# Kernel tuning notes

Measured on AMD Instinct MI355X. Metric: run time of the kernel, lower is better.

## Reference

```python
import jax, jax.numpy as jnp
import numpy as np

KERNEL = 5
DILATION = 2
PAD = DILATION * (KERNEL - 1) // 2  # symmetric 'same' padding along the conv axis


def _conv(x, w, b, padding, rhs_dilation):
    y = jax.lax.conv_general_dilated(
        x, w, window_strides=(1, 1), padding=padding,
        rhs_dilation=rhs_dilation,
        dimension_numbers=("NCHW", "OIHW", "NCHW"))
    return y + b[None, :, None, None]


def h_transform(x):
    # shear: [B,C,H,W] -> [B,C,H,2W-1], row i shifted right by i
    B, C, H, W = x.shape
    x = jnp.pad(x, ((0, 0), (0, 0), (0, 0), (0, W)))
    x = x.reshape(B, C, -1)[..., :-W]
    return x.reshape(B, C, H, 2 * W - 1)


def inv_h_transform(x):
    # inverse shear, assumes input [B,C,H,2H-1] -> [B,C,H,H]
    B, C, H, _ = x.shape
    x = x.reshape(B, C, -1)
    x = jnp.pad(x, ((0, 0), (0, 0), (0, H)))
    return x.reshape(B, C, H, 2 * H)[..., :H]


def v_transform(x):
    return jnp.transpose(h_transform(jnp.transpose(x, (0, 1, 3, 2))), (0, 1, 3, 2))


def inv_v_transform(x):
    return jnp.transpose(inv_h_transform(jnp.transpose(x, (0, 1, 3, 2))), (0, 1, 3, 2))


def setup_inputs() -> dict:
    key = jax.random.key(0)
    ks = jax.random.split(key, 9)
    B, C, H, W = 8, 256, 128, 128
    outc = C // 4
    x = jax.random.normal(ks[0], (B, C, H, W), dtype=jnp.float32)
    w_h = jax.random.normal(ks[1], (outc, C, 1, KERNEL), dtype=jnp.float32) * 0.02
    b_h = jax.random.normal(ks[2], (outc,), dtype=jnp.float32) * 0.02
    w_v = jax.random.normal(ks[3], (outc, C, KERNEL, 1), dtype=jnp.float32) * 0.02
    b_v = jax.random.normal(ks[4], (outc,), dtype=jnp.float32) * 0.02
    w_d1 = jax.random.normal(ks[5], (outc, C, KERNEL, 1), dtype=jnp.float32) * 0.02
    b_d1 = jax.random.normal(ks[6], (outc,), dtype=jnp.float32) * 0.02
    w_d2 = jax.random.normal(ks[7], (outc, C, 1, KERNEL), dtype=jnp.float32) * 0.02
    b_d2 = jax.random.normal(ks[8], (outc,), dtype=jnp.float32) * 0.02
    return {"x": x, "w_h": w_h, "b_h": b_h, "w_v": w_v, "b_v": b_v,
            "w_d1": w_d1, "b_d1": b_d1, "w_d2": w_d2, "b_d2": b_d2}


def reference(x, w_h, b_h, w_v, b_v, w_d1, b_d1, w_d2, b_d2):
    # branch 1: horizontal dilated conv (1,k)
    x1 = _conv(x, w_h, b_h, padding=((0, 0), (PAD, PAD)), rhs_dilation=(1, DILATION))
    # branch 2: vertical dilated conv (k,1)
    x2 = _conv(x, w_v, b_v, padding=((PAD, PAD), (0, 0)), rhs_dilation=(DILATION, 1))
    # branch 3: diagonal via h-shear + vertical conv + inverse shear
    x3 = inv_h_transform(_conv(h_transform(x), w_d1, b_d1,
                                padding=((PAD, PAD), (0, 0)), rhs_dilation=(DILATION, 1)))
    # branch 4: anti-diagonal via v-shear + horizontal conv + inverse shear
    x4 = inv_v_transform(_conv(v_transform(x), w_d2, b_d2,
                                padding=((0, 0), (PAD, PAD)), rhs_dilation=(1, DILATION)))
    return jnp.concatenate([x1, x2, x3, x4], axis=1)
```

## Files before the change

kernel.cpp:

```cpp
#include <hip/hip_runtime.h>
#include <hip/hip_bf16.h>


typedef __attribute__((ext_vector_type(8))) __bf16 bf16x8;
typedef __attribute__((ext_vector_type(4))) float f32x4;

#define HH 128
#define WW 128
#define CIN 256
#define NCHUNK 8
#define CHUNK 32
#define COLS 136
#define XS_ELEMS (5*COLS*CHUNK)
#define WPG (40*64*32)

__device__ __forceinline__ ushort f2bf(float f) {
    union { float f; unsigned u; } v; v.f = f;
    unsigned r = v.u + 0x7FFF + ((v.u >> 16) & 1);
    return (ushort)(r >> 16);
}

__global__ void repack_w(const float* __restrict__ w0, const float* __restrict__ w1,
                         const float* __restrict__ w2, const float* __restrict__ w3,
                         ushort* __restrict__ wp) {
    int idx = blockIdx.x * 256 + threadIdx.x;
    int g   = idx / WPG;
    int rem = idx - g * WPG;
    int s   = rem >> 11;
    int r2  = rem & 2047;
    int m   = r2 >> 5;
    int kk  = r2 & 31;
    int k   = s % 5;
    int cc  = s / 5;
    const float* w = (g == 0) ? w0 : (g == 1) ? w1 : (g == 2) ? w2 : w3;
    wp[idx] = f2bf(w[(m * CIN + cc * 32 + kk) * 5 + k]);
}

__global__ __launch_bounds__(256, 4)
void asterisk_mfma(const float* __restrict__ x,
                   const ushort* __restrict__ wp,
                   const float* __restrict__ b0, const float* __restrict__ b1,
                   const float* __restrict__ b2, const float* __restrict__ b3,
                   float* __restrict__ out) {
    __shared__ __align__(16) short xs[XS_ELEMS];

    const int t    = threadIdx.x;
    const int lane = t & 63;
    const int wid  = t >> 6;
    const int m16  = lane & 15;
    const int h    = lane >> 4;

    int id = blockIdx.x;
    int sw = (id & 7) * 128 + (id >> 3);
    const int b = sw >> 7;
    const int i = sw & 127;

    for (int e = t; e < 5 * 8 * CHUNK; e += 256) {
        int r  = e >> 8;
        int pc = (e >> 5) & 7;
        int c  = e & 31;
        int col = (pc < 4) ? pc : 128 + pc;
        xs[(r * COLS + col) * CHUNK + c] = 0;
    }
    for (int r = 0; r < 5; ++r) {
        int row = i + 2 * r - 4;
        if ((unsigned)row >= HH) {
            for (int e = t; e < COLS * CHUNK; e += 256)
                xs[r * COLS * CHUNK + e] = 0;
        }
    }

    const float* bias = (wid == 0) ? b0 : (wid == 1) ? b1 : (wid == 2) ? b2 : b3;
    f32x4 acc[4][8];
#pragma unroll
    for (int mb = 0; mb < 4; ++mb) {
        f32x4 bv;
#pragma unroll
        for (int rr = 0; rr < 4; ++rr) bv[rr] = bias[mb * 16 + h * 4 + rr];
#pragma unroll
        for (int nb = 0; nb < 8; ++nb) acc[mb][nb] = bv;
    }

    const int cg = t >> 5;
    const int q  = t & 31;
    const float* xb = x + (size_t)b * CIN * HH * WW;
    const ushort* wg = wp + (size_t)wid * WPG;

    for (int cc = 0; cc < NCHUNK; ++cc) {
        __syncthreads();
        {
            int c0 = cc * CHUNK + cg * 4;
            int slot = cg >> 1;
            int sub  = (cg & 1) * 4;
            const float* srcc = xb + (size_t)c0 * HH * WW + q * 4;
#pragma unroll
            for (int r = 0; r < 5; ++r) {
                int row = i + 2 * r - 4;
                if ((unsigned)row < HH) {
                    const float* src = srcc + (size_t)row * WW;
                    float4 v0 = *(const float4*)(src);
                    float4 v1 = *(const float4*)(src + HH * WW);
                    float4 v2 = *(const float4*)(src + 2 * HH * WW);
                    float4 v3 = *(const float4*)(src + 3 * HH * WW);
#pragma unroll
                    for (int jj = 0; jj < 4; ++jj) {
                        int col = q * 4 + 4 + jj;
                        int sl  = slot ^ ((col >> 2) & 3);
                        float f0 = ((const float*)&v0)[jj];
                        float f1 = ((const float*)&v1)[jj];
                        float f2 = ((const float*)&v2)[jj];
                        float f3 = ((const float*)&v3)[jj];
                        __hip_bfloat162 lo = __float22bfloat162_rn(make_float2(f0, f1));
                        __hip_bfloat162 hi = __float22bfloat162_rn(make_float2(f2, f3));
                        uint2 pk;
                        pk.x = *(unsigned*)&lo;
                        pk.y = *(unsigned*)&hi;
                        int wi = (r * COLS + col) * CHUNK + sl * 8 + sub;
                        wi ^= ((col >> 4) & 1) << 5;
                        *(uint2*)&xs[wi] = pk;
                    }
                }
            }
        }
        __syncthreads();
        const ushort* wc = wg + (size_t)(cc * 5 * 64 * 32) + m16 * 32 + h * 8;
        bf16x8 a_cur[4], a_nxt[4];
#pragma unroll
        for (int mb = 0; mb < 4; ++mb)
            a_cur[mb] = *(const bf16x8*)(wc + mb * 16 * 32);
#pragma unroll
        for (int k = 0; k < 5; ++k) {
            if (k < 4) {
                const ushort* wk1 = wc + (size_t)(k + 1) * 64 * 32;
#pragma unroll
                for (int mb = 0; mb < 4; ++mb)
                    a_nxt[mb] = *(const bf16x8*)(wk1 + mb * 16 * 32);
            }
            int r  = (wid == 0) ? 2 : (wid == 3 ? 4 - k : k);
            int dj = (wid == 1) ? 0 : (wid == 2 ? 4 - 2 * k : 2 * k - 4);
            int col0 = m16 + dj + 4;
            int sl   = h ^ ((col0 >> 2) & 3);
            int base = (r * COLS + col0) * CHUNK + sl * 8;
            base ^= ((col0 >> 4) & 1) << 5;
#pragma unroll
            for (int nb = 0; nb < 8; ++nb) {
                int idx = (base + nb * 16 * CHUNK) ^ ((nb & 1) << 5);
                bf16x8 bf = *(const bf16x8*)(&xs[idx]);
#pragma unroll
                for (int mb = 0; mb < 4; ++mb)
                    acc[mb][nb] = __builtin_amdgcn_mfma_f32_16x16x32_bf16(
                        a_cur[mb], bf, acc[mb][nb], 0, 0, 0);
            }
            if (k < 4) {
#pragma unroll
                for (int mb = 0; mb < 4; ++mb) a_cur[mb] = a_nxt[mb];
            }
        }
    }

    size_t obase = (((size_t)b * 256 + wid * 64) * HH + i) * WW;
#pragma unroll
    for (int mb = 0; mb < 4; ++mb)
#pragma unroll
        for (int rr = 0; rr < 4; ++rr) {
            float* op = out + obase + (size_t)(mb * 16 + h * 4 + rr) * HH * WW + m16;
#pragma unroll
            for (int nb = 0; nb < 8; ++nb)
                op[nb * 16] = acc[mb][nb][rr];
        }
}

extern "C" void kernel_launch(void* const* d_in, const int* in_sizes, int n_in,
                              void* d_out, int out_size, void* d_ws, size_t ws_size,
                              hipStream_t stream) {
    const float* x    = (const float*)d_in[0];
    const float* w_h  = (const float*)d_in[1];
    const float* b_h  = (const float*)d_in[2];
    const float* w_v  = (const float*)d_in[3];
    const float* b_v  = (const float*)d_in[4];
    const float* w_d1 = (const float*)d_in[5];
    const float* b_d1 = (const float*)d_in[6];
    const float* w_d2 = (const float*)d_in[7];
    const float* b_d2 = (const float*)d_in[8];
    float* out = (float*)d_out;
    ushort* wpack = (ushort*)d_ws;

    repack_w<<<1280, 256, 0, stream>>>(w_h, w_v, w_d1, w_d2, wpack);
    asterisk_mfma<<<1024, 256, 0, stream>>>(x, wpack, b_h, b_v, b_d1, b_d2, out);
}
```

Before: 120.4 us.

## Pre-convert input to swizzled bf16 planes and double-buffer LDS via global_load_lds

Adds a prep kernel that converts x once into bf16 tiles already in the swizzled LDS layout. The main kernel then stages each channel chunk with direct global-to-LDS 16-byte loads into a double buffer, so the next chunk's load overlaps the current chunk's MFMAs. Each 512-thread block computes two output rows that share a 6-row halo instead of 5 rows per single row, which cuts redundant input traffic. The cost is an extra kernel launch plus a full bf16 copy of x written to and read back from the workspace, and the larger block roughly halves the number of workgroups.

```diff
diff --git a/kernel.cpp b/kernel.cpp
--- a/kernel.cpp
+++ b/kernel.cpp
@@ -11,13 +11,22 @@
 #define NCHUNK 8
 #define CHUNK 32
 #define COLS 136
-#define XS_ELEMS (5*COLS*CHUNK)
+#define TROWS 6
+#define BUF_SHORTS (TROWS*COLS*CHUNK)
 #define WPG (40*64*32)
+#define XT_OFF (1u<<20)
+#define XT_BYTES (8u*128u*8u*8192u)
 
 __device__ __forceinline__ ushort f2bf(float f) {
     union { float f; unsigned u; } v; v.f = f;
     unsigned r = v.u + 0x7FFF + ((v.u >> 16) & 1);
     return (ushort)(r >> 16);
+}
+
+__device__ __forceinline__ void gll16(const void* g, const void* l) {
+    __builtin_amdgcn_global_load_lds(
+        (const __attribute__((address_space(1))) unsigned*)g,
+        (__attribute__((address_space(3))) unsigned*)l, 16, 0, 0);
 }
 
 __global__ void repack_w(const float* __restrict__ w0, const float* __restrict__ w1,
@@ -36,25 +45,179 @@
     wp[idx] = f2bf(w[(m * CIN + cc * 32 + kk) * 5 + k]);
 }
 
+__global__ void prep_x(const float* __restrict__ x, ushort* __restrict__ xt) {
+    int plane = blockIdx.x;
+    int cc  = plane & 7;
+    int row = (plane >> 3) & 127;
+    int b   = plane >> 10;
+    ushort* P = xt + (size_t)plane * 4096;
+    const float* xb = x + (((size_t)b * CIN + cc * CHUNK) * HH + row) * WW;
+    int t = threadIdx.x;
+#pragma unroll
+    for (int it = 0; it < 4; ++it) {
+        int id  = t + it * 256;
+        int c   = (id >> 7) * 4;
+        int col = id & 127;
+        float f0 = xb[(size_t)(c + 0) * (HH*WW) + col];
+        float f1 = xb[(size_t)(c + 1) * (HH*WW) + col];
+        float f2 = xb[(size_t)(c + 2) * (HH*WW) + col];
+        float f3 = xb[(size_t)(c + 3) * (HH*WW) + col];
+        __hip_bfloat162 lo = __float22bfloat162_rn(make_float2(f0, f1));
+        __hip_bfloat162 hi = __float22bfloat162_rn(make_float2(f2, f3));
+        uint2 pk;
+        pk.x = *(unsigned*)&lo;
+        pk.y = *(unsigned*)&hi;
+        int pc  = col + 4;
+        int idx = pc * 32 + (((c >> 3) ^ ((pc >> 2) & 3)) * 8) + (c & 7);
+        idx = (idx ^ (((pc >> 4) & 1) << 5)) - 128;
+        *(uint2*)&P[idx] = pk;
+    }
+}
+
+__global__ __launch_bounds__(512, 2)
+void asterisk_mfma2(const ushort* __restrict__ xt,
+                    const ushort* __restrict__ wp,
+                    const float* __restrict__ b0, const float* __restrict__ b1,
+                    const float* __restrict__ b2, const float* __restrict__ b3,
+                    float* __restrict__ out) {
+    __shared__ __align__(16) short xs[2][BUF_SHORTS];
+
+    const int t    = threadIdx.x;
+    const int lane = t & 63;
+    const int wid  = t >> 6;
+    const int g    = wid & 3;
+    const int l    = wid >> 2;
+    const int m16  = lane & 15;
+    const int h    = lane >> 4;
+
+    int id = blockIdx.x;
+    int sw = (id & 7) * 64 + (id >> 3);
+    const int b  = sw >> 6;
+    const int p  = sw & 63;
+    const int i0 = 4 * (p >> 1) + (p & 1);
+    const int i  = i0 + 2 * l;
+
+    for (int e = t; e < 2 * TROWS * 8 * CHUNK; e += 512) {
+        int s    = e;
+        int bufi = s >= TROWS * 8 * CHUNK;
+        if (bufi) s -= TROWS * 8 * CHUNK;
+        int r  = s >> 8;
+        int pc = (s >> 5) & 7;
+        int c  = s & 31;
+        int col = (pc < 4) ? pc : 128 + pc;
+        xs[bufi][(r * COLS + col) * CHUNK + c] = 0;
+    }
+    for (int r = 0; r < TROWS; ++r) {
+        int row = i0 + 2 * r - 4;
+        if ((unsigned)row >= HH) {
+            for (int e = t; e < 128 * CHUNK; e += 512) {
+                xs[0][(r * COLS + 4) * CHUNK + e] = 0;
+                xs[1][(r * COLS + 4) * CHUNK + e] = 0;
+            }
+        }
+    }
+
+    const float* bias = (g == 0) ? b0 : (g == 1) ? b1 : (g == 2) ? b2 : b3;
+    f32x4 acc[4][8];
+#pragma unroll
+    for (int mb = 0; mb < 4; ++mb) {
+        f32x4 bv;
+#pragma unroll
+        for (int rr = 0; rr < 4; ++rr) bv[rr] = bias[mb * 16 + h * 4 + rr];
+#pragma unroll
+        for (int nb = 0; nb < 8; ++nb) acc[mb][nb] = bv;
+    }
+
+    const ushort* wg = wp + (size_t)g * WPG;
+    const size_t pbase = (size_t)b * 128 * 8;
+
+    auto stage = [&](int cc, int sel) {
+#pragma unroll
+        for (int r = 0; r < TROWS; ++r) {
+            int row = i0 + 2 * r - 4;
+            if ((unsigned)row < HH) {
+                const ushort* gsrc = xt + (pbase + (size_t)row * 8 + cc) * 4096
+                                        + wid * 512 + lane * 8;
+                const short* ldst = &xs[sel][(r * COLS + 4) * CHUNK + wid * 512];
+                gll16(gsrc, ldst);
+            }
+        }
+    };
+
+    stage(0, 0);
+    __syncthreads();
+
+    for (int cc = 0; cc < NCHUNK; ++cc) {
+        const int sel = cc & 1;
+        if (cc < NCHUNK - 1) stage(cc + 1, sel ^ 1);
+
+        const short* xsel = xs[sel];
+        const ushort* wc = wg + (size_t)(cc * 5 * 64 * 32) + m16 * 32 + h * 8;
+        bf16x8 a_cur[4], a_nxt[4];
+#pragma unroll
+        for (int mb = 0; mb < 4; ++mb)
+            a_cur[mb] = *(const bf16x8*)(wc + mb * 16 * 32);
+#pragma unroll
+        for (int k = 0; k < 5; ++k) {
+            if (k < 4) {
+                const ushort* wk1 = wc + (size_t)(k + 1) * 64 * 32;
+#pragma unroll
+                for (int mb = 0; mb < 4; ++mb)
+                    a_nxt[mb] = *(const bf16x8*)(wk1 + mb * 16 * 32);
+            }
+            int rbase = (g == 0) ? 2 : (g == 3 ? 4 - k : k);
+            int r  = rbase + l;
+            int dj = (g == 1) ? 0 : (g == 2 ? 4 - 2 * k : 2 * k - 4);
+            int col0 = m16 + dj + 4;
+            int sl   = h ^ ((col0 >> 2) & 3);
+            int base = (r * COLS + col0) * CHUNK + sl * 8;
+            base ^= ((col0 >> 4) & 1) << 5;
+#pragma unroll
+            for (int nb = 0; nb < 8; ++nb) {
+                int idx = (base + nb * 16 * CHUNK) ^ ((nb & 1) << 5);
+                bf16x8 bf = *(const bf16x8*)(&xsel[idx]);
+#pragma unroll
+                for (int mb = 0; mb < 4; ++mb)
+                    acc[mb][nb] = __builtin_amdgcn_mfma_f32_16x16x32_bf16(
+                        a_cur[mb], bf, acc[mb][nb], 0, 0, 0);
+            }
+            if (k < 4) {
+#pragma unroll
+                for (int mb = 0; mb < 4; ++mb) a_cur[mb] = a_nxt[mb];
+            }
+        }
+        __syncthreads();
+    }
+
+    size_t obase = (((size_t)b * 256 + g * 64) * HH + i) * WW;
+#pragma unroll
+    for (int mb = 0; mb < 4; ++mb)
+#pragma unroll
+        for (int rr = 0; rr < 4; ++rr) {
+            float* op = out + obase + (size_t)(mb * 16 + h * 4 + rr) * HH * WW + m16;
+#pragma unroll
+            for (int nb = 0; nb < 8; ++nb)
+                op[nb * 16] = acc[mb][nb][rr];
+        }
+}
+
+#define XS_ELEMS (5*COLS*CHUNK)
 __global__ __launch_bounds__(256, 4)
-void asterisk_mfma(const float* __restrict__ x,
-                   const ushort* __restrict__ wp,
-                   const float* __restrict__ b0, const float* __restrict__ b1,
-                   const float* __restrict__ b2, const float* __restrict__ b3,
-                   float* __restrict__ out) {
+void asterisk_mfma_fb(const float* __restrict__ x,
+                      const ushort* __restrict__ wp,
+                      const float* __restrict__ b0, const float* __restrict__ b1,
+                      const float* __restrict__ b2, const float* __restrict__ b3,
+                      float* __restrict__ out) {
     __shared__ __align__(16) short xs[XS_ELEMS];
-
     const int t    = threadIdx.x;
     const int lane = t & 63;
     const int wid  = t >> 6;
     const int m16  = lane & 15;
     const int h    = lane >> 4;
-
     int id = blockIdx.x;
     int sw = (id & 7) * 128 + (id >> 3);
     const int b = sw >> 7;
     const int i = sw & 127;
-
     for (int e = t; e < 5 * 8 * CHUNK; e += 256) {
         int r  = e >> 8;
         int pc = (e >> 5) & 7;
@@ -64,12 +227,10 @@
     }
     for (int r = 0; r < 5; ++r) {
         int row = i + 2 * r - 4;
-        if ((unsigned)row >= HH) {
+        if ((unsigned)row >= HH)
             for (int e = t; e < COLS * CHUNK; e += 256)
                 xs[r * COLS * CHUNK + e] = 0;
-        }
-    }
-
+    }
     const float* bias = (wid == 0) ? b0 : (wid == 1) ? b1 : (wid == 2) ? b2 : b3;
     f32x4 acc[4][8];
 #pragma unroll
@@ -80,12 +241,10 @@
 #pragma unroll
         for (int nb = 0; nb < 8; ++nb) acc[mb][nb] = bv;
     }
-
     const int cg = t >> 5;
     const int q  = t & 31;
     const float* xb = x + (size_t)b * CIN * HH * WW;
     const ushort* wg = wp + (size_t)wid * WPG;
-
     for (int cc = 0; cc < NCHUNK; ++cc) {
         __syncthreads();
         {
@@ -157,7 +316,6 @@
             }
         }
     }
-
     size_t obase = (((size_t)b * 256 + wid * 64) * HH + i) * WW;
 #pragma unroll
     for (int mb = 0; mb < 4; ++mb)
@@ -186,5 +344,12 @@
     ushort* wpack = (ushort*)d_ws;
 
     repack_w<<<1280, 256, 0, stream>>>(w_h, w_v, w_d1, w_d2, wpack);
-    asterisk_mfma<<<1024, 256, 0, stream>>>(x, wpack, b_h, b_v, b_d1, b_d2, out);
-}
+
+    if (ws_size >= (size_t)XT_OFF + (size_t)XT_BYTES) {
+        ushort* xt = (ushort*)((char*)d_ws + XT_OFF);
+        prep_x<<<8192, 256, 0, stream>>>(x, xt);
+        asterisk_mfma2<<<512, 512, 0, stream>>>(xt, wpack, b_h, b_v, b_d1, b_d2, out);
+    } else {
+        asterisk_mfma_fb<<<1024, 256, 0, stream>>>(x, wpack, b_h, b_v, b_d1, b_d2, out);
+    }
+}
```

After: 149.7 us, median of 2. 24.4% more time.
